# Performance work log

Measured on AMD Instinct MI355X. Metric: run time of the kernel, lower is better.

Reference implementation:

```python
import jax, jax.numpy as jnp
import numpy as np

D_MODEL = 512
NUM_HEADS = 8
HEAD_DIM = D_MODEL // NUM_HEADS
ATTN_WINDOW = 256


def setup_inputs() -> dict:
    key = jax.random.key(0)
    ks = jax.random.split(key, 5)
    B, S = 2, 4096
    x = jax.random.normal(ks[0], (B, S, D_MODEL), dtype=jnp.float32)
    s = 1.0 / np.sqrt(D_MODEL)
    qkv_w = jax.random.uniform(ks[1], (3 * D_MODEL, D_MODEL), minval=-s, maxval=s, dtype=jnp.float32)
    qkv_b = jax.random.uniform(ks[2], (3 * D_MODEL,), minval=-s, maxval=s, dtype=jnp.float32)
    out_w = jax.random.uniform(ks[3], (D_MODEL, D_MODEL), minval=-s, maxval=s, dtype=jnp.float32)
    out_b = jax.random.uniform(ks[4], (D_MODEL,), minval=-s, maxval=s, dtype=jnp.float32)
    return {"x": x, "qkv_w": qkv_w, "qkv_b": qkv_b, "out_w": out_w, "out_b": out_b}


def reference(x, qkv_w, qkv_b, out_w, out_b):
    B, S, D = x.shape
    scale = HEAD_DIM ** (-0.5)
    qkv = x @ qkv_w.T + qkv_b                       # [B,S,3D]
    qkv = qkv.reshape(B, S, 3, NUM_HEADS, HEAD_DIM)
    q, k, v = qkv[:, :, 0], qkv[:, :, 1], qkv[:, :, 2]
    scores = jnp.einsum('bthd,bshd->bhts', q, k) * scale  # [B,H,S,S]
    i = jnp.arange(S)[:, None]
    j = jnp.arange(S)[None, :]
    # causal AND within sliding window of size ATTN_WINDOW
    mask = (j <= i) & (j >= i - ATTN_WINDOW)        # [S,S] bool
    scores = jnp.where(mask, scores, -jnp.inf)
    weights = jax.nn.softmax(scores, axis=-1)
    out = jnp.einsum('bhts,bshd->bthd', weights, v).reshape(B, S, D)
    return out @ out_w.T + out_b
```

## Files before the change

### kernel.cpp

```cpp
#include <hip/hip_runtime.h>

#define S_LEN 4096
#define BATCH 2
#define DM 512
#define NH 8
#define DH 64
#define WINDOW 256

typedef __bf16 bf16x8 __attribute__((ext_vector_type(8)));
typedef float f32x4 __attribute__((ext_vector_type(4)));
typedef unsigned short u16x8 __attribute__((ext_vector_type(8)));

typedef const __attribute__((address_space(1))) unsigned int* gas_ptr;
typedef __attribute__((address_space(3))) unsigned int* las_ptr;

#define SCALE_LOG2E 0.1803368801111204f
#define FIXED_MAX 16.0f

__device__ __forceinline__ unsigned short b16(float f) {
  __bf16 h = (__bf16)f;
  return __builtin_bit_cast(unsigned short, h);
}

#define N4_X (8192 * 512 / 4)
#define N4_QW (1536 * 512 / 4)
#define N4_OW (512 * 512 / 4)
__global__ __launch_bounds__(256) void convert_all(const float* __restrict__ x,
                                                   const float* __restrict__ qw,
                                                   const float* __restrict__ ow,
                                                   unsigned short* __restrict__ dst) {
  const int i = blockIdx.x * blockDim.x + threadIdx.x;
  const float4* src;
  int off;
  if (i < N4_X) { src = (const float4*)x; off = 0; }
  else if (i < N4_X + N4_QW) { src = (const float4*)qw; off = N4_X; }
  else { src = (const float4*)ow; off = N4_X + N4_QW; }
  const float4 v = src[i - off];
  ushort4 o;
  o.x = b16(v.x); o.y = b16(v.y); o.z = b16(v.z); o.w = b16(v.w);
  ((ushort4*)dst)[i] = o;
}

__device__ __forceinline__ void gemm_core(const unsigned short* __restrict__ A,
                                          const unsigned short* __restrict__ Bm,
                                          int m0, int n0,
                                          unsigned short* sA, unsigned short* sB,
                                          f32x4 acc[4][4]) {
  const int t = threadIdx.x;
  const int wave = t >> 6, lane = t & 63;
  const int wr = wave >> 1, wc = wave & 1;
  const int quad = lane >> 4, l16 = lane & 15;

  for (int k0 = 0; k0 < 512; k0 += 32) {
#pragma unroll
    for (int p = 0; p < 2; ++p) {
      const int ci = wave * 128 + p * 64 + lane;
      const int row = ci >> 2, cg = ci & 3;
      const unsigned short* ga = A + (size_t)(m0 + row) * 512 + k0 + cg * 8;
      __builtin_amdgcn_global_load_lds((gas_ptr)(const void*)ga,
                                       (las_ptr)(void*)(sA + wave * 1024 + p * 512), 16, 0, 0);
      const unsigned short* gb = Bm + (size_t)(n0 + row) * 512 + k0 + cg * 8;
      __builtin_amdgcn_global_load_lds((gas_ptr)(const void*)gb,
                                       (las_ptr)(void*)(sB + wave * 1024 + p * 512), 16, 0, 0);
    }
    __syncthreads();
    bf16x8 af[4], bff[4];
#pragma unroll
    for (int i = 0; i < 4; ++i)
      af[i] = *(const bf16x8*)&sA[(wr * 64 + i * 16 + l16) * 32 + quad * 8];
#pragma unroll
    for (int j = 0; j < 4; ++j)
      bff[j] = *(const bf16x8*)&sB[(wc * 64 + j * 16 + l16) * 32 + quad * 8];
#pragma unroll
    for (int i = 0; i < 4; ++i)
#pragma unroll
      for (int j = 0; j < 4; ++j)
        acc[i][j] = __builtin_amdgcn_mfma_f32_16x16x32_bf16(af[i], bff[j], acc[i][j], 0, 0, 0);
    __syncthreads();
  }
}

__global__ __launch_bounds__(256) void gemm_qkv(const unsigned short* __restrict__ xb,
                                                const unsigned short* __restrict__ wb,
                                                const float* __restrict__ bias,
                                                unsigned short* __restrict__ Qb,
                                                unsigned short* __restrict__ Kb,
                                                unsigned short* __restrict__ Vt) {
  __shared__ __align__(16) unsigned short sA[128 * 32];
  __shared__ __align__(16) unsigned short sB[128 * 32];
  f32x4 acc[4][4] = {};
  const int id = blockIdx.x;
  const int X = id & 7;
  const int t2 = id >> 3;
  const int cb = t2 % 12;
  const int rb = (t2 / 12) * 8 + X;
  const int m0 = rb * 128, n0 = cb * 128;
  gemm_core(xb, wb, m0, n0, sA, sB, acc);

  const int t = threadIdx.x;
  const int wave = t >> 6, lane = t & 63;
  const int wr = wave >> 1, wc = wave & 1;
  const int quad = lane >> 4, l16 = lane & 15;
#pragma unroll
  for (int j = 0; j < 4; ++j) {
    const int n = n0 + wc * 64 + j * 16 + l16;
    const float bv = bias[n];
#pragma unroll
    for (int i = 0; i < 4; ++i) {
      const int mr = m0 + wr * 64 + i * 16 + quad * 4;
      if (n < DM) {
#pragma unroll
        for (int r = 0; r < 4; ++r)
          Qb[(size_t)(mr + r) * DM + n] = b16((acc[i][j][r] + bv) * SCALE_LOG2E);
      } else if (n < 2 * DM) {
#pragma unroll
        for (int r = 0; r < 4; ++r)
          Kb[(size_t)(mr + r) * DM + (n - DM)] = b16(acc[i][j][r] + bv);
      } else {
        const int d = n & 63, h = (n - 2 * DM) >> 6;
#pragma unroll
        for (int r = 0; r < 4; ++r) {
          const int m = mr + r;
          const int b = m >> 12, s = m & (S_LEN - 1);
          Vt[((size_t)((b * NH + h) * DH + d)) * S_LEN + s] = b16(acc[i][j][r] + bv);
        }
      }
    }
  }
}

__global__ __launch_bounds__(256) void gemm_out(const unsigned short* __restrict__ Ab,
                                                const unsigned short* __restrict__ wb,
                                                const float* __restrict__ bias,
                                                float* __restrict__ C) {
  __shared__ __align__(16) unsigned short sA[64 * 32];
  __shared__ __align__(16) unsigned short sB[128 * 32];
  const int t = threadIdx.x;
  const int wave = t >> 6, lane = t & 63;
  const int wr = wave >> 1, wc = wave & 1;
  const int quad = lane >> 4, l16 = lane & 15;
  const int id = blockIdx.x;
  const int X = id & 7;
  const int t2 = id >> 3;
  const int cb = t2 % 4;
  const int rb = (t2 / 4) * 8 + X;
  const int m0 = rb * 64, n0 = cb * 128;

  f32x4 acc[2][4] = {};
  for (int k0 = 0; k0 < 512; k0 += 32) {
    {
      const int row = t >> 2, cg = t & 3;
      const unsigned short* ga = Ab + (size_t)(m0 + row) * 512 + k0 + cg * 8;
      __builtin_amdgcn_global_load_lds((gas_ptr)(const void*)ga,
                                       (las_ptr)(void*)(sA + wave * 512), 16, 0, 0);
    }
#pragma unroll
    for (int p = 0; p < 2; ++p) {
      const int ci = wave * 128 + p * 64 + lane;
      const int row = ci >> 2, cg = ci & 3;
      const unsigned short* gb = wb + (size_t)(n0 + row) * 512 + k0 + cg * 8;
      __builtin_amdgcn_global_load_lds((gas_ptr)(const void*)gb,
                                       (las_ptr)(void*)(sB + wave * 1024 + p * 512), 16, 0, 0);
    }
    __syncthreads();
    bf16x8 af[2], bff[4];
#pragma unroll
    for (int i = 0; i < 2; ++i)
      af[i] = *(const bf16x8*)&sA[(wr * 32 + i * 16 + l16) * 32 + quad * 8];
#pragma unroll
    for (int j = 0; j < 4; ++j)
      bff[j] = *(const bf16x8*)&sB[(wc * 64 + j * 16 + l16) * 32 + quad * 8];
#pragma unroll
    for (int i = 0; i < 2; ++i)
#pragma unroll
      for (int j = 0; j < 4; ++j)
        acc[i][j] = __builtin_amdgcn_mfma_f32_16x16x32_bf16(af[i], bff[j], acc[i][j], 0, 0, 0);
    __syncthreads();
  }

#pragma unroll
  for (int j = 0; j < 4; ++j) {
    const int n = n0 + wc * 64 + j * 16 + l16;
    const float bv = bias[n];
#pragma unroll
    for (int i = 0; i < 2; ++i) {
      const int mr = m0 + wr * 32 + i * 16 + quad * 4;
#pragma unroll
      for (int r = 0; r < 4; ++r)
        C[(size_t)(mr + r) * DM + n] = acc[i][j][r] + bv;
    }
  }
}

__global__ __launch_bounds__(256) void attn_mfma(const unsigned short* __restrict__ Qb,
                                                 const unsigned short* __restrict__ Kb,
                                                 const unsigned short* __restrict__ Vt,
                                                 unsigned short* __restrict__ AO) {
  __shared__ __align__(16) unsigned short Ks[64 * 72];
  __shared__ __align__(16) unsigned short Vs[64 * 72];
  __shared__ __align__(16) unsigned short Ps[64 * 72];
  const int t = threadIdx.x;
  const int wave = t >> 6, lane = t & 63;
  const int quad = lane >> 4, l16 = lane & 15;

  const int id = blockIdx.x;
  const int X = id & 7;
  const int o = (id >> 3) & 7;
  const int h = (id >> 6) & 7;
  const int b = id >> 9;
  const int g = (X - h) & 7;
  const int qt = g * 8 + o;
  const int q0 = qt * 64;

  const unsigned short* Kbase = Kb + (size_t)b * S_LEN * DM + h * DH;
  const unsigned short* Vbase = Vt + (size_t)((b * NH + h) * DH) * S_LEN;

  const unsigned short* qrow =
      Qb + (size_t)(b * S_LEN + q0 + wave * 16 + l16) * DM + h * DH;
  const bf16x8 aq0 = *(const bf16x8*)(qrow + quad * 8);
  const bf16x8 aq1 = *(const bf16x8*)(qrow + 32 + quad * 8);

  const int first = (qt >= 4) ? 0 : (4 - qt);

  u16x8 kbuf[2][2], vbuf[2][2];
#define LOAD_CHUNK(c0, p)                                                      \
  do {                                                                         \
    _Pragma("unroll") for (int s = 0; s < 2; ++s) {                            \
      const int f = t + 256 * s;                                               \
      const int row = f >> 3, c8 = f & 7;                                      \
      kbuf[p][s] = *(const u16x8*)(Kbase + (size_t)((c0) + row) * DM + c8 * 8);\
      vbuf[p][s] = *(const u16x8*)(Vbase + (size_t)row * S_LEN + (c0) + c8 * 8);\
    }                                                                          \
  } while (0)

#pragma unroll
  for (int c = 0; c < 5; ++c)
    if (c == first) LOAD_CHUNK(q0 - WINDOW + c * 64, c & 1);

  float l_ = 0.f;
  f32x4 O[4] = {};

#pragma unroll
  for (int c = 0; c < 5; ++c) {
    if (c < first) continue;
    const int c0 = q0 - WINDOW + c * 64;
    __syncthreads();
#pragma unroll
    for (int s = 0; s < 2; ++s) {
      const int f = t + 256 * s;
      const int row = f >> 3, c8 = f & 7;
      *(u16x8*)&Ks[row * 72 + c8 * 8] = kbuf[c & 1][s];
      *(u16x8*)&Vs[row * 72 + c8 * 8] = vbuf[c & 1][s];
    }
    if (c < 4) LOAD_CHUNK(c0 + 64, (c + 1) & 1);
    __syncthreads();

    f32x4 sc[4];
#pragma unroll
    for (int nt = 0; nt < 4; ++nt) {
      bf16x8 bk0 = *(const bf16x8*)&Ks[(nt * 16 + l16) * 72 + quad * 8];
      bf16x8 bk1 = *(const bf16x8*)&Ks[(nt * 16 + l16) * 72 + 32 + quad * 8];
      f32x4 z = {};
      z = __builtin_amdgcn_mfma_f32_16x16x32_bf16(bk0, aq0, z, 0, 0, 0);
      sc[nt] = __builtin_amdgcn_mfma_f32_16x16x32_bf16(bk1, aq1, z, 0, 0, 0);
    }

    const int iiq = wave * 16 + l16;
#pragma unroll
    for (int nt = 0; nt < 4; ++nt) {
#pragma unroll
      for (int r = 0; r < 4; ++r) {
        const int jjk = nt * 16 + quad * 4 + r;
        float p = exp2f(sc[nt][r] - FIXED_MAX);
        if (c == 0) p = (jjk >= iiq) ? p : 0.f;
        if (c == 4) p = (jjk <= iiq) ? p : 0.f;
        sc[nt][r] = p;
        l_ += p;
      }
      ushort4 pk;
      pk.x = b16(sc[nt][0]);
      pk.y = b16(sc[nt][1]);
      pk.z = b16(sc[nt][2]);
      pk.w = b16(sc[nt][3]);
      *(ushort4*)&Ps[(wave * 16 + l16) * 72 + nt * 16 + quad * 4] = pk;
    }

    const bf16x8 bp0 = *(const bf16x8*)&Ps[(wave * 16 + l16) * 72 + quad * 8];
    const bf16x8 bp1 = *(const bf16x8*)&Ps[(wave * 16 + l16) * 72 + 32 + quad * 8];

#pragma unroll
    for (int nt = 0; nt < 4; ++nt) {
      bf16x8 bv0 = *(const bf16x8*)&Vs[(nt * 16 + l16) * 72 + quad * 8];
      bf16x8 bv1 = *(const bf16x8*)&Vs[(nt * 16 + l16) * 72 + 32 + quad * 8];
      O[nt] = __builtin_amdgcn_mfma_f32_16x16x32_bf16(bv0, bp0, O[nt], 0, 0, 0);
      O[nt] = __builtin_amdgcn_mfma_f32_16x16x32_bf16(bv1, bp1, O[nt], 0, 0, 0);
    }
  }

  l_ += __shfl_xor(l_, 16);
  l_ += __shfl_xor(l_, 32);
  const float linv = 1.f / l_;

  unsigned short* aoRow =
      AO + (size_t)(b * S_LEN + q0 + wave * 16 + l16) * DM + h * DH;
#pragma unroll
  for (int nt = 0; nt < 4; ++nt) {
    ushort4 o4;
    o4.x = b16(O[nt][0] * linv);
    o4.y = b16(O[nt][1] * linv);
    o4.z = b16(O[nt][2] * linv);
    o4.w = b16(O[nt][3] * linv);
    *(ushort4*)(aoRow + nt * 16 + quad * 4) = o4;
  }
}

extern "C" void kernel_launch(void* const* d_in, const int* in_sizes, int n_in,
                              void* d_out, int out_size, void* d_ws, size_t ws_size,
                              hipStream_t stream) {
  const float* x = (const float*)d_in[0];
  const float* qkv_w = (const float*)d_in[1];
  const float* qkv_b = (const float*)d_in[2];
  const float* out_w = (const float*)d_in[3];
  const float* out_b = (const float*)d_in[4];
  float* out = (float*)d_out;

  const int M = BATCH * S_LEN;
  unsigned short* ws = (unsigned short*)d_ws;
  unsigned short* xb   = ws;
  unsigned short* wqkv = xb + (size_t)M * DM;
  unsigned short* wout = wqkv + 3 * DM * DM;
  unsigned short* Qb   = wout + DM * DM;
  unsigned short* Kb   = Qb + (size_t)M * DM;
  unsigned short* Vt   = Kb + (size_t)M * DM;
  unsigned short* AO   = Vt + (size_t)M * DM;

  convert_all<<<(N4_X + N4_QW + N4_OW) / 256, 256, 0, stream>>>(x, qkv_w, out_w, xb);

  gemm_qkv<<<768, 256, 0, stream>>>(xb, wqkv, qkv_b, Qb, Kb, Vt);

  attn_mfma<<<1024, 256, 0, stream>>>(Qb, Kb, Vt, AO);

  gemm_out<<<512, 256, 0, stream>>>(AO, wout, out_b, out);
}
```

Baseline: 127.1 us.

## Double-buffer LDS with async global-to-LDS loads in GEMMs and attention

Both GEMM kernels now double-buffer their LDS tiles. They issue the next k-slice's global_load_lds before computing on the current one, and use explicit vmcnt waits with raw barriers. The attention kernel drops its register-staged K/V copies in favour of direct global-to-LDS loads into double buffers, with an XOR-swizzled 64-wide layout in place of 72-element padding. The goal is to overlap memory latency with MFMA work and cut LDS store traffic. The cost is doubled LDS use and fragile hand-counted vmcnt values.

```diff
diff --git a/kernel.cpp b/kernel.cpp
--- a/kernel.cpp
+++ b/kernel.cpp
@@ -9,13 +9,20 @@
 
 typedef __bf16 bf16x8 __attribute__((ext_vector_type(8)));
 typedef float f32x4 __attribute__((ext_vector_type(4)));
-typedef unsigned short u16x8 __attribute__((ext_vector_type(8)));
 
 typedef const __attribute__((address_space(1))) unsigned int* gas_ptr;
 typedef __attribute__((address_space(3))) unsigned int* las_ptr;
 
 #define SCALE_LOG2E 0.1803368801111204f
 #define FIXED_MAX 16.0f
+
+#define BAR()                                   \
+  do {                                          \
+    asm volatile("" ::: "memory");              \
+    __builtin_amdgcn_s_barrier();               \
+    asm volatile("" ::: "memory");              \
+  } while (0)
+#define WAITVM(N) asm volatile("s_waitcnt vmcnt(" #N ")" ::: "memory")
 
 __device__ __forceinline__ unsigned short b16(float f) {
   __bf16 h = (__bf16)f;
@@ -51,33 +58,49 @@
   const int wr = wave >> 1, wc = wave & 1;
   const int quad = lane >> 4, l16 = lane & 15;
 
+#define QKV_STAGE(k0, buf)                                                       \
+  do {                                                                           \
+    _Pragma("unroll") for (int p = 0; p < 2; ++p) {                              \
+      const int ci = wave * 128 + p * 64 + lane;                                 \
+      const int row = ci >> 2, cg = ci & 3;                                      \
+      const unsigned short* ga = A + (size_t)(m0 + row) * 512 + (k0) + cg * 8;   \
+      __builtin_amdgcn_global_load_lds(                                          \
+          (gas_ptr)(const void*)ga,                                              \
+          (las_ptr)(void*)(sA + (buf) * 4096 + wave * 1024 + p * 512), 16, 0, 0);\
+      const unsigned short* gb = Bm + (size_t)(n0 + row) * 512 + (k0) + cg * 8;  \
+      __builtin_amdgcn_global_load_lds(                                          \
+          (gas_ptr)(const void*)gb,                                              \
+          (las_ptr)(void*)(sB + (buf) * 4096 + wave * 1024 + p * 512), 16, 0, 0);\
+    }                                                                            \
+  } while (0)
+
+  QKV_STAGE(0, 0);
   for (int k0 = 0; k0 < 512; k0 += 32) {
-#pragma unroll
-    for (int p = 0; p < 2; ++p) {
-      const int ci = wave * 128 + p * 64 + lane;
-      const int row = ci >> 2, cg = ci & 3;
-      const unsigned short* ga = A + (size_t)(m0 + row) * 512 + k0 + cg * 8;
-      __builtin_amdgcn_global_load_lds((gas_ptr)(const void*)ga,
-                                       (las_ptr)(void*)(sA + wave * 1024 + p * 512), 16, 0, 0);
-      const unsigned short* gb = Bm + (size_t)(n0 + row) * 512 + k0 + cg * 8;
-      __builtin_amdgcn_global_load_lds((gas_ptr)(const void*)gb,
-                                       (las_ptr)(void*)(sB + wave * 1024 + p * 512), 16, 0, 0);
-    }
-    __syncthreads();
+    const int cur = (k0 >> 5) & 1;
+    BAR();
+    if (k0 + 32 < 512) {
+      QKV_STAGE(k0 + 32, cur ^ 1);
+      WAITVM(4);
+    } else {
+      WAITVM(0);
+    }
+    BAR();
+    const unsigned short* bA = sA + cur * 4096;
+    const unsigned short* bB = sB + cur * 4096;
     bf16x8 af[4], bff[4];
 #pragma unroll
     for (int i = 0; i < 4; ++i)
-      af[i] = *(const bf16x8*)&sA[(wr * 64 + i * 16 + l16) * 32 + quad * 8];
+      af[i] = *(const bf16x8*)&bA[(wr * 64 + i * 16 + l16) * 32 + quad * 8];
 #pragma unroll
     for (int j = 0; j < 4; ++j)
-      bff[j] = *(const bf16x8*)&sB[(wc * 64 + j * 16 + l16) * 32 + quad * 8];
+      bff[j] = *(const bf16x8*)&bB[(wc * 64 + j * 16 + l16) * 32 + quad * 8];
 #pragma unroll
     for (int i = 0; i < 4; ++i)
 #pragma unroll
       for (int j = 0; j < 4; ++j)
         acc[i][j] = __builtin_amdgcn_mfma_f32_16x16x32_bf16(af[i], bff[j], acc[i][j], 0, 0, 0);
-    __syncthreads();
-  }
+  }
+#undef QKV_STAGE
 }
 
 __global__ __launch_bounds__(256) void gemm_qkv(const unsigned short* __restrict__ xb,
@@ -86,8 +109,8 @@
                                                 unsigned short* __restrict__ Qb,
                                                 unsigned short* __restrict__ Kb,
                                                 unsigned short* __restrict__ Vt) {
-  __shared__ __align__(16) unsigned short sA[128 * 32];
-  __shared__ __align__(16) unsigned short sB[128 * 32];
+  __shared__ __align__(16) unsigned short sA[2 * 128 * 32];
+  __shared__ __align__(16) unsigned short sB[2 * 128 * 32];
   f32x4 acc[4][4] = {};
   const int id = blockIdx.x;
   const int X = id & 7;
@@ -133,8 +156,8 @@
                                                 const unsigned short* __restrict__ wb,
                                                 const float* __restrict__ bias,
                                                 float* __restrict__ C) {
-  __shared__ __align__(16) unsigned short sA[64 * 32];
-  __shared__ __align__(16) unsigned short sB[128 * 32];
+  __shared__ __align__(16) unsigned short sA[2 * 64 * 32];
+  __shared__ __align__(16) unsigned short sB[2 * 128 * 32];
   const int t = threadIdx.x;
   const int wave = t >> 6, lane = t & 63;
   const int wr = wave >> 1, wc = wave & 1;
@@ -146,37 +169,53 @@
   const int rb = (t2 / 4) * 8 + X;
   const int m0 = rb * 64, n0 = cb * 128;
 
+#define OUT_STAGE(k0, buf)                                                       \
+  do {                                                                           \
+    {                                                                            \
+      const int row = t >> 2, cg = t & 3;                                        \
+      const unsigned short* ga = Ab + (size_t)(m0 + row) * 512 + (k0) + cg * 8;  \
+      __builtin_amdgcn_global_load_lds(                                          \
+          (gas_ptr)(const void*)ga,                                              \
+          (las_ptr)(void*)(sA + (buf) * 2048 + wave * 512), 16, 0, 0);           \
+    }                                                                            \
+    _Pragma("unroll") for (int p = 0; p < 2; ++p) {                              \
+      const int ci = wave * 128 + p * 64 + lane;                                 \
+      const int row = ci >> 2, cg = ci & 3;                                      \
+      const unsigned short* gb = wb + (size_t)(n0 + row) * 512 + (k0) + cg * 8;  \
+      __builtin_amdgcn_global_load_lds(                                          \
+          (gas_ptr)(const void*)gb,                                              \
+          (las_ptr)(void*)(sB + (buf) * 4096 + wave * 1024 + p * 512), 16, 0, 0);\
+    }                                                                            \
+  } while (0)
+
   f32x4 acc[2][4] = {};
+  OUT_STAGE(0, 0);
   for (int k0 = 0; k0 < 512; k0 += 32) {
-    {
-      const int row = t >> 2, cg = t & 3;
-      const unsigned short* ga = Ab + (size_t)(m0 + row) * 512 + k0 + cg * 8;
-      __builtin_amdgcn_global_load_lds((gas_ptr)(const void*)ga,
-                                       (las_ptr)(void*)(sA + wave * 512), 16, 0, 0);
-    }
-#pragma unroll
-    for (int p = 0; p < 2; ++p) {
-      const int ci = wave * 128 + p * 64 + lane;
-      const int row = ci >> 2, cg = ci & 3;
-      const unsigned short* gb = wb + (size_t)(n0 + row) * 512 + k0 + cg * 8;
-      __builtin_amdgcn_global_load_lds((gas_ptr)(const void*)gb,
-                                       (las_ptr)(void*)(sB + wave * 1024 + p * 512), 16, 0, 0);
-    }
-    __syncthreads();
+    const int cur = (k0 >> 5) & 1;
+    BAR();
+    if (k0 + 32 < 512) {
+      OUT_STAGE(k0 + 32, cur ^ 1);
+      WAITVM(3);
+    } else {
+      WAITVM(0);
+    }
+    BAR();
+    const unsigned short* bA = sA + cur * 2048;
+    const unsigned short* bB = sB + cur * 4096;
     bf16x8 af[2], bff[4];
 #pragma unroll
     for (int i = 0; i < 2; ++i)
-      af[i] = *(const bf16x8*)&sA[(wr * 32 + i * 16 + l16) * 32 + quad * 8];
+      af[i] = *(const bf16x8*)&bA[(wr * 32 + i * 16 + l16) * 32 + quad * 8];
 #pragma unroll
     for (int j = 0; j < 4; ++j)
-      bff[j] = *(const bf16x8*)&sB[(wc * 64 + j * 16 + l16) * 32 + quad * 8];
+      bff[j] = *(const bf16x8*)&bB[(wc * 64 + j * 16 + l16) * 32 + quad * 8];
 #pragma unroll
     for (int i = 0; i < 2; ++i)
 #pragma unroll
       for (int j = 0; j < 4; ++j)
         acc[i][j] = __builtin_amdgcn_mfma_f32_16x16x32_bf16(af[i], bff[j], acc[i][j], 0, 0, 0);
-    __syncthreads();
-  }
+  }
+#undef OUT_STAGE
 
 #pragma unroll
   for (int j = 0; j < 4; ++j) {
@@ -196,9 +235,9 @@
                                                  const unsigned short* __restrict__ Kb,
                                                  const unsigned short* __restrict__ Vt,
                                                  unsigned short* __restrict__ AO) {
-  __shared__ __align__(16) unsigned short Ks[64 * 72];
-  __shared__ __align__(16) unsigned short Vs[64 * 72];
-  __shared__ __align__(16) unsigned short Ps[64 * 72];
+  __shared__ __align__(16) unsigned short Ks[2 * 64 * 64];
+  __shared__ __align__(16) unsigned short Vs[2 * 64 * 64];
+  __shared__ __align__(16) unsigned short Ps[64 * 64];
   const int t = threadIdx.x;
   const int wave = t >> 6, lane = t & 63;
   const int quad = lane >> 4, l16 = lane & 15;
@@ -222,50 +261,67 @@
 
   const int first = (qt >= 4) ? 0 : (4 - qt);
 
-  u16x8 kbuf[2][2], vbuf[2][2];
-#define LOAD_CHUNK(c0, p)                                                      \
-  do {                                                                         \
-    _Pragma("unroll") for (int s = 0; s < 2; ++s) {                            \
-      const int f = t + 256 * s;                                               \
-      const int row = f >> 3, c8 = f & 7;                                      \
-      kbuf[p][s] = *(const u16x8*)(Kbase + (size_t)((c0) + row) * DM + c8 * 8);\
-      vbuf[p][s] = *(const u16x8*)(Vbase + (size_t)row * S_LEN + (c0) + c8 * 8);\
-    }                                                                          \
+  int grow[2], gcol[2];
+#pragma unroll
+  for (int s = 0; s < 2; ++s) {
+    const int L = t + 256 * s;
+    grow[s] = L >> 3;
+    gcol[s] = ((L & 7) ^ (grow[s] & 7)) * 8;
+  }
+
+#define ATTN_STAGE(c0, buf)                                                       \
+  do {                                                                            \
+    _Pragma("unroll") for (int s = 0; s < 2; ++s) {                               \
+      const unsigned short* gk = Kbase + (size_t)((c0) + grow[s]) * DM + gcol[s]; \
+      __builtin_amdgcn_global_load_lds(                                           \
+          (gas_ptr)(const void*)gk,                                               \
+          (las_ptr)(void*)(Ks + (buf) * 4096 + wave * 512 + s * 2048), 16, 0, 0); \
+      const unsigned short* gv = Vbase + (size_t)grow[s] * S_LEN + (c0) + gcol[s];\
+      __builtin_amdgcn_global_load_lds(                                           \
+          (gas_ptr)(const void*)gv,                                               \
+          (las_ptr)(void*)(Vs + (buf) * 4096 + wave * 512 + s * 2048), 16, 0, 0); \
+    }                                                                             \
   } while (0)
 
-#pragma unroll
-  for (int c = 0; c < 5; ++c)
-    if (c == first) LOAD_CHUNK(q0 - WINDOW + c * 64, c & 1);
+  ATTN_STAGE(q0 - WINDOW + first * 64, first & 1);
 
   float l_ = 0.f;
   f32x4 O[4] = {};
+
+  const int sw = l16 & 7;
+  const int c0q = (quad ^ sw) * 8;
+  const int c1q = ((quad | 4) ^ sw) * 8;
 
 #pragma unroll
   for (int c = 0; c < 5; ++c) {
     if (c < first) continue;
     const int c0 = q0 - WINDOW + c * 64;
-    __syncthreads();
-#pragma unroll
-    for (int s = 0; s < 2; ++s) {
-      const int f = t + 256 * s;
-      const int row = f >> 3, c8 = f & 7;
-      *(u16x8*)&Ks[row * 72 + c8 * 8] = kbuf[c & 1][s];
-      *(u16x8*)&Vs[row * 72 + c8 * 8] = vbuf[c & 1][s];
-    }
-    if (c < 4) LOAD_CHUNK(c0 + 64, (c + 1) & 1);
-    __syncthreads();
+    const int cur = c & 1;
+    BAR();
+    if (c < 4) {
+      ATTN_STAGE(c0 + 64, cur ^ 1);
+      WAITVM(4);
+    } else {
+      WAITVM(0);
+    }
+    BAR();
+
+    const unsigned short* Kc = Ks + cur * 4096;
+    const unsigned short* Vc = Vs + cur * 4096;
 
     f32x4 sc[4];
 #pragma unroll
     for (int nt = 0; nt < 4; ++nt) {
-      bf16x8 bk0 = *(const bf16x8*)&Ks[(nt * 16 + l16) * 72 + quad * 8];
-      bf16x8 bk1 = *(const bf16x8*)&Ks[(nt * 16 + l16) * 72 + 32 + quad * 8];
+      const int krow = (nt * 16 + l16) * 64;
+      bf16x8 bk0 = *(const bf16x8*)&Kc[krow + c0q];
+      bf16x8 bk1 = *(const bf16x8*)&Kc[krow + c1q];
       f32x4 z = {};
       z = __builtin_amdgcn_mfma_f32_16x16x32_bf16(bk0, aq0, z, 0, 0, 0);
       sc[nt] = __builtin_amdgcn_mfma_f32_16x16x32_bf16(bk1, aq1, z, 0, 0, 0);
     }
 
     const int iiq = wave * 16 + l16;
+    const int prow = iiq * 64;
 #pragma unroll
     for (int nt = 0; nt < 4; ++nt) {
 #pragma unroll
@@ -282,20 +338,22 @@
       pk.y = b16(sc[nt][1]);
       pk.z = b16(sc[nt][2]);
       pk.w = b16(sc[nt][3]);
-      *(ushort4*)&Ps[(wave * 16 + l16) * 72 + nt * 16 + quad * 4] = pk;
-    }
-
-    const bf16x8 bp0 = *(const bf16x8*)&Ps[(wave * 16 + l16) * 72 + quad * 8];
-    const bf16x8 bp1 = *(const bf16x8*)&Ps[(wave * 16 + l16) * 72 + 32 + quad * 8];
+      *(ushort4*)&Ps[prow + (((nt * 2 + (quad >> 1)) ^ sw) * 8) + (quad & 1) * 4] = pk;
+    }
+
+    const bf16x8 bp0 = *(const bf16x8*)&Ps[prow + c0q];
+    const bf16x8 bp1 = *(const bf16x8*)&Ps[prow + c1q];
 
 #pragma unroll
     for (int nt = 0; nt < 4; ++nt) {
-      bf16x8 bv0 = *(const bf16x8*)&Vs[(nt * 16 + l16) * 72 + quad * 8];
-      bf16x8 bv1 = *(const bf16x8*)&Vs[(nt * 16 + l16) * 72 + 32 + quad * 8];
+      const int vrow = (nt * 16 + l16) * 64;
+      bf16x8 bv0 = *(const bf16x8*)&Vc[vrow + c0q];
+      bf16x8 bv1 = *(const bf16x8*)&Vc[vrow + c1q];
       O[nt] = __builtin_amdgcn_mfma_f32_16x16x32_bf16(bv0, bp0, O[nt], 0, 0, 0);
       O[nt] = __builtin_amdgcn_mfma_f32_16x16x32_bf16(bv1, bp1, O[nt], 0, 0, 0);
     }
   }
+#undef ATTN_STAGE
 
   l_ += __shfl_xor(l_, 16);
   l_ += __shfl_xor(l_, 32);
```

Result: no change. 127.6 us (+0.4%).
